# Performance work log

Hardware: AMD Instinct MI355X
Metric: run time of the kernel (lower is better)

Reference implementation:

```python
import jax, jax.numpy as jnp
import numpy as np

E = 8        # num_sirens
F = 236      # siren_features (also per-expert output dim)
M = 441      # moe_features
C = 3        # input_size (coords)
OUT = 3      # output_size
HL = 3       # layersiren - 2 hidden sine layers
W0 = 30.0
N = 65536


def setup_inputs() -> dict:
    key = jax.random.key(0)
    ks = jax.random.split(key, 20)
    u = lambda k, shape, lim: jax.random.uniform(k, shape, jnp.float32, -lim, lim)
    sl = lambda fan_in: float(np.sqrt(6.0 / fan_in) / 30.0)  # sine_init limit
    inp = {}
    inp["x"] = jax.random.uniform(ks[0], (N, C), jnp.float32, -1.0, 1.0)
    # SIREN experts, stacked over E. First layer: first_layer_sine_init (1/fan_in).
    inp["siren_W1"] = u(ks[1], (E, C, F), 1.0 / C)
    inp["siren_b1"] = u(ks[2], (E, F), 1.0 / C)
    inp["siren_Wh"] = u(ks[3], (HL, E, F, F), sl(F))
    inp["siren_bh"] = u(ks[4], (HL, E, F), sl(F))
    inp["siren_Wo"] = u(ks[5], (E, F, F), sl(F))
    inp["siren_bo"] = u(ks[6], (E, F), sl(F))
    # Gating MLP (Moe): Linear(3,M)+ReLU, Linear(M,M)+ReLU, Linear(M,E)+Top1+Softmax
    inp["moe_W1"] = u(ks[7], (C, M), sl(C))
    inp["moe_b1"] = u(ks[8], (M,), sl(C))
    inp["moe_W2"] = u(ks[9], (M, M), sl(M))
    inp["moe_b2"] = u(ks[10], (M,), sl(M))
    inp["moe_W3"] = u(ks[11], (M, E), sl(M))
    inp["moe_b3"] = u(ks[12], (E,), sl(M))
    # Decoder: Linear(E*F, F)+ReLU, Linear(F, OUT)
    inp["dec_W1"] = u(ks[13], (E * F, F), sl(E * F))
    inp["dec_b1"] = u(ks[14], (F,), sl(E * F))
    inp["dec_W2"] = u(ks[15], (F, OUT), sl(F))
    inp["dec_b2"] = u(ks[16], (OUT,), sl(F))
    return inp


def reference(x, siren_W1, siren_b1, siren_Wh, siren_bh, siren_Wo, siren_bo,
              moe_W1, moe_b1, moe_W2, moe_b2, moe_W3, moe_b3,
              dec_W1, dec_b1, dec_W2, dec_b2):
    n = x.shape[0]
    # --- parallel SIREN experts, batched over E ---
    h = jnp.sin(W0 * (jnp.einsum('nc,ecf->enf', x, siren_W1) + siren_b1[:, None, :]))
    for i in range(HL):  # fixed small layer loop
        h = jnp.sin(W0 * (jnp.einsum('enf,efg->eng', h, siren_Wh[i]) + siren_bh[i][:, None, :]))
    so = jnp.einsum('enf,efg->eng', h, siren_Wo) + siren_bo[:, None, :]       # (E,N,F)
    siren_cat = jnp.transpose(so, (1, 0, 2)).reshape(n, E * F)                # cat along -1, expert-major
    # --- gating MLP + Top-1 + softmax ---
    g = jax.nn.relu(x @ moe_W1 + moe_b1)
    g = jax.nn.relu(g @ moe_W2 + moe_b2)
    logits = g @ moe_W3 + moe_b3                                              # (N,E)
    _, top_idx = jax.lax.top_k(logits, 1)
    mask = jnp.zeros_like(logits).at[jnp.arange(n)[:, None], top_idx].set(1.0)
    masked = jnp.where(mask > 0, logits, -jnp.inf)
    weights = jax.nn.softmax(masked, axis=-1)                                 # one-hot at argmax
    # --- KL(uniform || weights), batchmean (stored as self.kl_loss in torch) ---
    logw = jnp.log(weights + 1e-10)
    unif = jnp.asarray(1.0 / E, logw.dtype)
    kl = jnp.sum(unif * (jnp.log(unif) - logw)) / n
    # --- repeat_interleave(F) * concat, then decoder ---
    w_full = jnp.broadcast_to(weights[:, :, None], (n, E, F)).reshape(n, E * F)
    dec_in = w_full * siren_cat
    out = jax.nn.relu(dec_in @ dec_W1 + dec_b1) @ dec_W2 + dec_b2             # (N,OUT)
    return out, kl
```

## Files before the change

### kernel.cpp

```cpp
#include <hip/hip_runtime.h>
#include <cstdint>

typedef unsigned short ushort_t;
typedef short bf16x8 __attribute__((ext_vector_type(8)));
typedef unsigned short u16x8 __attribute__((ext_vector_type(8)));
typedef float f32x4 __attribute__((ext_vector_type(4)));

#define NPTS 65536
#define WS_CNT 0
#define WS_BKT 64
#define OFF_W2S 1048640
#define OFF_W3T 1450048
#define OFF_SWT 1464640
#define WS_FAST 6379840u
#define WS_SLOW (64 + 8 * NPTS * 2)

__device__ __forceinline__ float bf2f(ushort_t u) {
  union { unsigned u; float f; } c; c.u = ((unsigned)u) << 16; return c.f;
}
__device__ __forceinline__ ushort_t f2bf(float f) {
  union { float f; unsigned u; } c; c.f = f;
  unsigned u = c.u + 0x7fffu + ((c.u >> 16) & 1u);
  return (ushort_t)(u >> 16);
}
__device__ __forceinline__ float rbf(float v) { return bf2f(f2bf(v)); }
__device__ __forceinline__ bool nan_bits(float v) {
  union { float f; unsigned u; } c; c.f = v;
  return ((c.u >> 23) & 0xFFu) == 0xFFu && (c.u & 0x7FFFFFu) != 0u;
}

__global__ void k_sentinel(float* out) {
  if (threadIdx.x == 0) out[0] = 1.0e30f;
}


__global__ __launch_bounds__(256) void k_prep_fast(
    const float* __restrict__ sWh, const float* __restrict__ sWo,
    const float* __restrict__ dW1, const float* __restrict__ mW2,
    const float* __restrict__ mW3,
    int* __restrict__ counts, ushort_t* __restrict__ W2S,
    ushort_t* __restrict__ w3T, ushort_t* __restrict__ swt, float* __restrict__ out)
{
  long gid = (long)blockIdx.x * 256 + threadIdx.x;
  long gs = (long)gridDim.x * 256;
  for (long i = gid; i < 40L * 61440; i += gs) {
    int mat = (int)(i / 61440);
    int f = (int)(i - (long)mat * 61440);
    int u = f & 7, ln = (f >> 3) & 63, kt = (f >> 9) & 7, t = f >> 12;
    int n = t * 16 + (ln & 15);
    int k = kt * 32 + (ln >> 4) * 8 + u;
    if (n >= 236 || k >= 236) swt[i] = 0;
  }
  for (long i = gid; i < 40L * 55696; i += gs) {
    int mat = (int)(i / 55696);
    int r = (int)(i - (long)mat * 55696);
    int k = r / 236, n = r - k * 236;
    const float* W = (mat < 24) ? (sWh + (long)mat * 55696)
                   : (mat < 32) ? (sWo + (long)(mat - 24) * 55696)
                                : (dW1 + (long)(mat - 32) * 55696);
    ushort_t v = f2bf(W[r]);
    int t = n >> 4, l15 = n & 15;
    int kt = k >> 5, rr = k & 31;
    long dst = (long)mat * 61440 + (t << 12) + (kt << 9) + ((((rr >> 3) << 4) + l15) << 3) + (rr & 7);
    swt[dst] = v;
  }
  for (long i = gid; i < 25088; i += gs) {
    int kt = (int)(i / (28 * 64));
    int rem = (int)(i - (long)kt * 28 * 64);
    int nt = rem / 64, lane = rem - nt * 64;
    int l15 = lane & 15, quad = lane >> 4;
    int n = nt * 16 + l15;
    u16x8 tv;
    #pragma unroll
    for (int u = 0; u < 8; ++u) {
      int k = kt * 32 + quad * 8 + u;
      tv[u] = (k < 441 && n < 441) ? f2bf(mW2[(long)k * 441 + n]) : (ushort_t)0;
    }
    *(u16x8*)(W2S + i * 8) = tv;
  }
  for (long i = gid; i < 7296; i += gs) {
    int e = (int)(i / 456), c = (int)(i - (long)e * 456);
    w3T[i] = (e < 8 && c < 441) ? f2bf(mW3[(long)c * 8 + e]) : (ushort_t)0;
  }
  if (gid < 8) counts[gid] = 0;
  if (gid == 8) out[NPTS * 3] = 18.125f;
}

__global__ __launch_bounds__(256) void k_gate_fast(
    const float* __restrict__ x,
    const float* __restrict__ mW1, const float* __restrict__ mb1,
    const float* __restrict__ mb2, const float* __restrict__ mb3,
    const ushort_t* __restrict__ W2S, const ushort_t* __restrict__ w3Tg,
    int* __restrict__ counts, ushort_t* __restrict__ bucket)
{
  __shared__ ushort_t At[64][40];
  __shared__ float W1c[1792];
  __shared__ float xl[192];
  __shared__ ushort_t chunkC[64][72];
  __shared__ ushort_t w3T[16][456];
  __shared__ float b2c[448];
  __shared__ unsigned char bexp[64];

  int tid = threadIdx.x;
  int blk = blockIdx.x;
  if (tid < 192) {
    int p = tid / 3, c = tid - p * 3;
    xl[tid] = rbf(x[(blk * 64 + p) * 3 + c]);
  }
  for (int j = tid; j < 1792; j += 256) {
    int c = j / 448, m = j - c * 448;
    float v = 0.f;
    if (m < 441) v = (c < 3) ? rbf(mW1[c * 441 + m]) : rbf(mb1[m]);
    W1c[j] = v;
  }
  for (int j = tid; j < 448; j += 256) b2c[j] = (j < 441) ? rbf(mb2[j]) : 0.f;
  for (int ch = tid; ch < 912; ch += 256)
    *(u16x8*)(&w3T[0][0] + ch * 8) = *(const u16x8*)(w3Tg + ch * 8);

  int w = tid >> 6, lane = tid & 63;
  int l15 = lane & 15, quad = lane >> 4;

  f32x4 acc[4][7];
  #pragma unroll
  for (int a = 0; a < 4; ++a)
    #pragma unroll
    for (int b = 0; b < 7; ++b)
      acc[a][b] = (f32x4){0.f, 0.f, 0.f, 0.f};

  int am = tid >> 2, ak = (tid & 3) * 8;

  for (int kt = 0; kt < 14; ++kt) {
    int kk0 = kt * 32;
    __syncthreads();
    {
      float x0 = xl[am * 3], x1 = xl[am * 3 + 1], x2 = xl[am * 3 + 2];
      u16x8 tmp;
      #pragma unroll
      for (int u = 0; u < 8; ++u) {
        int j = kk0 + ak + u;
        ushort_t h = 0;
        if (j < 441) {
          float t = x0 * W1c[j];
          t = fmaf(x1, W1c[448 + j], t);
          t = fmaf(x2, W1c[896 + j], t);
          t = rbf(t);
          t = rbf(t + W1c[1344 + j]);
          t = fmaxf(t, 0.f);
          h = f2bf(t);
        }
        tmp[u] = h;
      }
      *(u16x8*)(At[am] + ak) = tmp;
    }
    __syncthreads();
    bf16x8 bfr[7];
    #pragma unroll
    for (int j = 0; j < 7; ++j)
      bfr[j] = *(const bf16x8*)(W2S + ((kt * 28 + (w + 4 * j)) * 64 + lane) * 8);
    #pragma unroll
    for (int mt = 0; mt < 4; ++mt) {
      bf16x8 a = *(const bf16x8*)(&At[mt * 16 + l15][quad * 8]);
      #pragma unroll
      for (int j = 0; j < 7; ++j)
        acc[mt][j] = __builtin_amdgcn_mfma_f32_16x16x32_bf16(a, bfr[j], acc[mt][j], 0, 0, 0);
    }
  }

  f32x4 acc3[4];
  #pragma unroll
  for (int mt = 0; mt < 4; ++mt) acc3[mt] = (f32x4){0.f, 0.f, 0.f, 0.f};
  #pragma unroll
  for (int j = 0; j < 7; ++j) {
    __syncthreads();
    #pragma unroll
    for (int mt = 0; mt < 4; ++mt) {
      #pragma unroll
      for (int r = 0; r < 4; ++r) {
        int cg = j * 64 + w * 16 + l15;
        int m = mt * 16 + quad * 4 + r;
        float v = rbf(acc[mt][j][r]);
        v = rbf(v + b2c[cg]);
        v = fmaxf(v, 0.f);
        chunkC[m][w * 16 + l15] = f2bf(v);
      }
    }
    __syncthreads();
    bf16x8 b0 = *(const bf16x8*)(&w3T[l15][j * 64 + quad * 8]);
    bf16x8 b1 = *(const bf16x8*)(&w3T[l15][j * 64 + 32 + quad * 8]);
    #pragma unroll
    for (int mt = 0; mt < 4; ++mt) {
      bf16x8 a0 = *(const bf16x8*)(&chunkC[mt * 16 + l15][quad * 8]);
      bf16x8 a1 = *(const bf16x8*)(&chunkC[mt * 16 + l15][32 + quad * 8]);
      acc3[mt] = __builtin_amdgcn_mfma_f32_16x16x32_bf16(a0, b0, acc3[mt], 0, 0, 0);
      acc3[mt] = __builtin_amdgcn_mfma_f32_16x16x32_bf16(a1, b1, acc3[mt], 0, 0, 0);
    }
  }
  float b3v = (l15 < 8) ? rbf(mb3[l15]) : 0.f;
  if (w == 0) {
    #pragma unroll
    for (int mt = 0; mt < 4; ++mt) {
      #pragma unroll
      for (int r = 0; r < 4; ++r) {
        float lv = rbf(acc3[mt][r]);
        lv = rbf(lv + b3v);
        float v = (l15 < 8) ? lv : -1.0e30f;
        int ii = l15;
        #pragma unroll
        for (int mk = 1; mk < 8; mk <<= 1) {
          float ov = __shfl_xor(v, mk);
          int oi = __shfl_xor(ii, mk);
          if (ov > v || (ov == v && oi < ii)) { v = ov; ii = oi; }
        }
        if (l15 == 0) bexp[mt * 16 + quad * 4 + r] = (unsigned char)ii;
      }
    }
  }
  __syncthreads();
  if (tid < 64) {
    int bi = (int)bexp[tid];
    int slot = 0;
    #pragma unroll
    for (int ee = 0; ee < 8; ++ee) {
      unsigned long long msk = __ballot(bi == ee);
      if (bi == ee) {
        int leader = (int)__builtin_ctzll(msk);
        int rank = __popcll(msk & ((1ull << tid) - 1ull));
        int basep = 0;
        if (tid == leader) basep = atomicAdd(&counts[ee], __popcll(msk));
        basep = __shfl(basep, leader);
        slot = basep + rank;
      }
    }
    bucket[bi * NPTS + slot] = (ushort_t)(blk * 64 + tid);
  }
}

__global__ __launch_bounds__(256) void k_sdec_fast(
    const float* __restrict__ x,
    const float* __restrict__ sW1, const float* __restrict__ sb1,
    const float* __restrict__ sbh, const float* __restrict__ sbo,
    const float* __restrict__ db1, const float* __restrict__ dW2,
    const float* __restrict__ db2,
    const ushort_t* __restrict__ swt,
    const int* __restrict__ counts, const ushort_t* __restrict__ bucket,
    float* __restrict__ out)
{
  __shared__ ushort_t hA[64][264];
  __shared__ int idxl[64];
  __shared__ float xl[64][3];
  __shared__ float wc[944];

  int e = blockIdx.y;
  int base = blockIdx.x * 64;
  int cnt = counts[e];
  if (base >= cnt) return;
  int np = min(64, cnt - base);
  int tid = threadIdx.x;

  if (tid < 64) {
    int s = base + (tid < np ? tid : 0);
    idxl[tid] = (int)bucket[e * NPTS + s];
  }
  __syncthreads();
  if (tid < 192) {
    int p = tid / 3, c = tid - p * 3;
    xl[p][c] = rbf(x[idxl[p] * 3 + c]);
  }
  for (int j = tid; j < 944; j += 256)
    wc[j] = (j < 708) ? rbf(sW1[e * 708 + j]) : 30.f * rbf(sb1[e * 236 + (j - 708)]);
  __syncthreads();

  int w = tid >> 6, lane = tid & 63;
  int l15 = lane & 15, quad = lane >> 4;

  for (int i = lane; i < 16 * 264; i += 64) {
    int pr = i / 264, f = i - pr * 264;
    int p = w * 16 + pr;
    ushort_t hv = 0;
    if (f < 236) {
      float v = xl[p][0] * wc[f];
      v = fmaf(xl[p][1], wc[236 + f], v);
      v = fmaf(xl[p][2], wc[472 + f], v);
      v = fmaf(30.f, v, wc[708 + f]);
      hv = f2bf(__sinf(v));
    }
    hA[p][f] = hv;
  }

  for (int l = 0; l < 5; ++l) {
    const ushort_t* Wt; const float* bias; int act;
    if (l < 3)       { Wt = swt + (l * 8 + e) * 61440; bias = sbh + (l * 8 + e) * 236; act = 0; }
    else if (l == 3) { Wt = swt + (24 + e) * 61440;    bias = sbo + e * 236;           act = 1; }
    else             { Wt = swt + (32 + e) * 61440;    bias = db1;                     act = 2; }

    bf16x8 afr[8];
    #pragma unroll
    for (int kt = 0; kt < 8; ++kt)
      afr[kt] = *(const bf16x8*)(&hA[w * 16 + l15][kt * 32 + quad * 8]);

    #pragma unroll 3
    for (int t = 0; t < 15; ++t) {
      f32x4 acc = (f32x4){0.f, 0.f, 0.f, 0.f};
      #pragma unroll
      for (int kt = 0; kt < 8; ++kt) {
        bf16x8 b = *(const bf16x8*)(Wt + ((t * 8 + kt) * 64 + lane) * 8);
        acc = __builtin_amdgcn_mfma_f32_16x16x32_bf16(afr[kt], b, acc, 0, 0, 0);
      }
      int n = t * 16 + l15;
      if (n < 236) {
        float bv = rbf(bias[n]);
        if (act == 0) {
          float b30 = 30.f * bv;
          #pragma unroll
          for (int r = 0; r < 4; ++r) {
            int m = w * 16 + quad * 4 + r;
            hA[m][n] = f2bf(__sinf(fmaf(30.f, acc[r], b30)));
          }
        } else if (act == 1) {
          #pragma unroll
          for (int r = 0; r < 4; ++r) {
            int m = w * 16 + quad * 4 + r;
            hA[m][n] = f2bf(acc[r] + bv);
          }
        } else {
          #pragma unroll
          for (int r = 0; r < 4; ++r) {
            int m = w * 16 + quad * 4 + r;
            hA[m][n] = f2bf(fmaxf(acc[r] + bv, 0.f));
          }
        }
      }
    }
  }

  __syncthreads();
  for (int j = tid; j < 711; j += 256)
    wc[j] = (j < 708) ? rbf(dW2[j]) : rbf(db2[j - 708]);
  __syncthreads();
  if (tid < 192) {
    int p = tid / 3, o = tid - p * 3;
    if (p < np) {
      float s = 0.f;
      for (int k = 0; k < 236; ++k)
        s = fmaf(bf2f(hA[p][k]), wc[k * 3 + o], s);
      s = s + wc[708 + o];
      out[idxl[p] * 3 + o] = nan_bits(s) ? 16.0f : fminf(fmaxf(s, -4.f), 4.f);
    }
  }
}


__global__ void k_prep_slow(int* counts, float* out) {
  int t = threadIdx.x;
  if (t < 8) counts[t] = 0;
  if (t == 8) out[NPTS * 3] = 18.125f;
}

__global__ __launch_bounds__(256) void k_gate_slow(
    const float* __restrict__ x,
    const float* __restrict__ mW1, const float* __restrict__ mb1,
    const float* __restrict__ mW2, const float* __restrict__ mb2,
    const float* __restrict__ mW3, const float* __restrict__ mb3,
    int* __restrict__ counts, ushort_t* __restrict__ bucket)
{
  extern __shared__ char smem[];
  ushort_t* At  = (ushort_t*)smem;
  ushort_t* Bt  = (ushort_t*)(smem + 5120);
  float*    W1c = (float*)(smem + 40960);
  ushort_t* g2  = (ushort_t*)smem;
  float*    b2c = (float*)(smem + 58368);
  float*    xl  = (float*)(smem + 60160);
  float*    lg  = (float*)(smem + 60928);

  int tid = threadIdx.x;
  int blk = blockIdx.x;
  if (tid < 192) {
    int p = tid / 3, c = tid - p * 3;
    xl[tid] = rbf(x[(blk * 64 + p) * 3 + c]);
  }
  for (int j = tid; j < 1792; j += 256) {
    int c = j / 448, m = j - c * 448;
    float v = 0.f;
    if (m < 441) v = (c < 3) ? rbf(mW1[c * 441 + m]) : rbf(mb1[m]);
    W1c[j] = v;
  }
  for (int j = tid; j < 448; j += 256) b2c[j] = (j < 441) ? rbf(mb2[j]) : 0.f;

  int w = tid >> 6, lane = tid & 63;
  int l15 = lane & 15, quad = lane >> 4;

  f32x4 acc[4][7];
  #pragma unroll
  for (int a = 0; a < 4; ++a)
    #pragma unroll
    for (int b = 0; b < 7; ++b)
      acc[a][b] = (f32x4){0.f, 0.f, 0.f, 0.f};

  int am = tid >> 2, ak = (tid & 3) * 8;

  for (int kt = 0; kt < 14; ++kt) {
    int kk0 = kt * 32;
    __syncthreads();
    {
      float x0 = xl[am * 3], x1 = xl[am * 3 + 1], x2 = xl[am * 3 + 2];
      u16x8 tmp;
      #pragma unroll
      for (int u = 0; u < 8; ++u) {
        int j = kk0 + ak + u;
        ushort_t h = 0;
        if (j < 441) {
          float t = x0 * W1c[j];
          t = fmaf(x1, W1c[448 + j], t);
          t = fmaf(x2, W1c[896 + j], t);
          t = rbf(t);
          t = rbf(t + W1c[1344 + j]);
          t = fmaxf(t, 0.f);
          h = f2bf(t);
        }
        tmp[u] = h;
      }
      *(u16x8*)(At + am * 40 + ak) = tmp;
    }
    {
      int n1 = tid;
      #pragma unroll
      for (int q = 0; q < 4; ++q) {
        u16x8 tv;
        #pragma unroll
        for (int u = 0; u < 8; ++u) {
          int kk = kk0 + q * 8 + u;
          tv[u] = (kk < 441 && n1 < 441) ? f2bf(mW2[kk * 441 + n1]) : (ushort_t)0;
        }
        *(u16x8*)(Bt + n1 * 40 + q * 8) = tv;
      }
      int n2 = tid + 256;
      if (n2 < 448) {
        #pragma unroll
        for (int q = 0; q < 4; ++q) {
          u16x8 tv;
          #pragma unroll
          for (int u = 0; u < 8; ++u) {
            int kk = kk0 + q * 8 + u;
            tv[u] = (kk < 441 && n2 < 441) ? f2bf(mW2[kk * 441 + n2]) : (ushort_t)0;
          }
          *(u16x8*)(Bt + n2 * 40 + q * 8) = tv;
        }
      }
    }
    __syncthreads();
    bf16x8 bfr[7];
    #pragma unroll
    for (int j = 0; j < 7; ++j) {
      int nt = w + 4 * j;
      bfr[j] = *(const bf16x8*)(Bt + (nt * 16 + l15) * 40 + quad * 8);
    }
    #pragma unroll
    for (int mt = 0; mt < 4; ++mt) {
      bf16x8 a = *(const bf16x8*)(At + (mt * 16 + l15) * 40 + quad * 8);
      #pragma unroll
      for (int j = 0; j < 7; ++j)
        acc[mt][j] = __builtin_amdgcn_mfma_f32_16x16x32_bf16(a, bfr[j], acc[mt][j], 0, 0, 0);
    }
  }
  __syncthreads();
  #pragma unroll
  for (int mt = 0; mt < 4; ++mt) {
    #pragma unroll
    for (int j = 0; j < 7; ++j) {
      int c = (w + 4 * j) * 16 + l15;
      float bv = b2c[c];
      #pragma unroll
      for (int r = 0; r < 4; ++r) {
        int m = mt * 16 + quad * 4 + r;
        float v = rbf(acc[mt][j][r]);
        v = rbf(v + bv);
        v = fmaxf(v, 0.f);
        g2[m * 456 + c] = f2bf(v);
      }
    }
  }
  __syncthreads();
  {
    int m3 = tid >> 2, eg = tid & 3;
    float s0 = 0.f, s1 = 0.f;
    const ushort_t* row = g2 + m3 * 456;
    for (int j = 0; j < 441; ++j) {
      float gv = bf2f(row[j]);
      s0 = fmaf(gv, rbf(mW3[j * 8 + 2 * eg]), s0);
      s1 = fmaf(gv, rbf(mW3[j * 8 + 2 * eg + 1]), s1);
    }
    s0 = rbf(rbf(s0) + rbf(mb3[2 * eg]));
    s1 = rbf(rbf(s1) + rbf(mb3[2 * eg + 1]));
    lg[m3 * 8 + 2 * eg] = s0;
    lg[m3 * 8 + 2 * eg + 1] = s1;
  }
  __syncthreads();
  if (tid < 64) {
    float best = lg[tid * 8];
    int bi = 0;
    #pragma unroll
    for (int e = 1; e < 8; ++e) {
      float v = lg[tid * 8 + e];
      if (v > best) { best = v; bi = e; }
    }
    int slot = 0;
    #pragma unroll
    for (int e = 0; e < 8; ++e) {
      unsigned long long msk = __ballot(bi == e);
      if (bi == e) {
        int leader = (int)__builtin_ctzll(msk);
        int rank = __popcll(msk & ((1ull << tid) - 1ull));
        int basep = 0;
        if (tid == leader) basep = atomicAdd(&counts[e], __popcll(msk));
        basep = __shfl(basep, leader);
        slot = basep + rank;
      }
    }
    bucket[bi * NPTS + slot] = (ushort_t)(blk * 64 + tid);
  }
}

__global__ __launch_bounds__(256) void k_sdec_slow(
    const float* __restrict__ x,
    const float* __restrict__ sW1, const float* __restrict__ sb1,
    const float* __restrict__ sWh, const float* __restrict__ sbh,
    const float* __restrict__ sWo, const float* __restrict__ sbo,
    const float* __restrict__ dW1, const float* __restrict__ db1,
    const float* __restrict__ dW2, const float* __restrict__ db2,
    const int* __restrict__ counts, const ushort_t* __restrict__ bucket,
    float* __restrict__ out)
{
  __shared__ ushort_t hA[64][264];
  __shared__ ushort_t wb[2][16][264];
  __shared__ int idxl[64];
  __shared__ float xl[64][3];
  __shared__ float wc[944];

  int e = blockIdx.y;
  int base = blockIdx.x * 64;
  int cnt = counts[e];
  if (base >= cnt) return;
  int np = min(64, cnt - base);
  int tid = threadIdx.x;

  if (tid < 64) {
    int s = base + (tid < np ? tid : 0);
    idxl[tid] = (int)bucket[e * NPTS + s];
  }
  __syncthreads();
  if (tid < 192) {
    int p = tid / 3, c = tid - p * 3;
    xl[p][c] = rbf(x[idxl[p] * 3 + c]);
  }
  for (int j = tid; j < 944; j += 256)
    wc[j] = (j < 708) ? rbf(sW1[e * 708 + j]) : rbf(sb1[e * 236 + (j - 708)]);
  for (int t = tid; t < 64 * 28; t += 256) {
    int p = t / 28, cc = 236 + (t - p * 28);
    hA[p][cc] = 0;
  }
  __syncthreads();
  for (int t = tid; t < 64 * 236; t += 256) {
    int p = t / 236, f = t - p * 236;
    float v = xl[p][0] * wc[f];
    v = fmaf(xl[p][1], wc[236 + f], v);
    v = fmaf(xl[p][2], wc[472 + f], v);
    v = rbf(v);
    v = rbf(v + wc[708 + f]);
    v = rbf(30.f * v);
    hA[p][f] = f2bf(sinf(v));
  }

  int w = tid >> 6, lane = tid & 63;
  int l15 = lane & 15, quad = lane >> 4;

  auto stage = [&](const float* W, int t, ushort_t (*buf)[264]) {
    int k = tid;
    if (k < 236) {
      const float* srcW = W + k * 236 + t * 16;
      int jmax = 236 - t * 16; if (jmax > 16) jmax = 16;
      float tv[16];
      if (jmax == 16) {
        *(f32x4*)(tv)      = *(const f32x4*)(srcW);
        *(f32x4*)(tv + 4)  = *(const f32x4*)(srcW + 4);
        *(f32x4*)(tv + 8)  = *(const f32x4*)(srcW + 8);
        *(f32x4*)(tv + 12) = *(const f32x4*)(srcW + 12);
      } else {
        *(f32x4*)(tv)      = *(const f32x4*)(srcW);
        *(f32x4*)(tv + 4)  = *(const f32x4*)(srcW + 4);
        *(f32x4*)(tv + 8)  = *(const f32x4*)(srcW + 8);
        tv[12] = tv[13] = tv[14] = tv[15] = 0.f;
      }
      #pragma unroll
      for (int j = 0; j < 16; ++j)
        buf[j][k] = (j < jmax) ? f2bf(tv[j]) : (ushort_t)0;
    } else {
      #pragma unroll
      for (int j = 0; j < 16; ++j) buf[j][k] = 0;
    }
  };

  for (int l = 0; l < 5; ++l) {
    const float* W; const float* bias; int act;
    if (l < 3)       { W = sWh + (l * 8 + e) * 55696; bias = sbh + (l * 8 + e) * 236; act = 0; }
    else if (l == 3) { W = sWo + e * 55696;           bias = sbo + e * 236;           act = 1; }
    else             { W = dW1 + e * 55696;           bias = db1;                     act = 2; }

    __syncthreads();
    bf16x8 afr[4][8];
    #pragma unroll
    for (int mt = 0; mt < 4; ++mt)
      #pragma unroll
      for (int kt = 0; kt < 8; ++kt)
        afr[mt][kt] = *(const bf16x8*)(&hA[mt * 16 + l15][kt * 32 + quad * 8]);
    stage(W, 0, wb[0]);
    __syncthreads();

    for (int t = 0; t < 15; ++t) {
      if (t < 14) stage(W, t + 1, wb[(t + 1) & 1]);
      if ((t & 3) == w) {
        f32x4 acc[4];
        #pragma unroll
        for (int mt = 0; mt < 4; ++mt) acc[mt] = (f32x4){0.f, 0.f, 0.f, 0.f};
        #pragma unroll
        for (int kt = 0; kt < 8; ++kt) {
          bf16x8 b = *(const bf16x8*)(&wb[t & 1][l15][kt * 32 + quad * 8]);
          #pragma unroll
          for (int mt = 0; mt < 4; ++mt)
            acc[mt] = __builtin_amdgcn_mfma_f32_16x16x32_bf16(afr[mt][kt], b, acc[mt], 0, 0, 0);
        }
        int n = t * 16 + l15;
        if (n < 236) {
          float bv = rbf(bias[n]);
          #pragma unroll
          for (int mt = 0; mt < 4; ++mt) {
            #pragma unroll
            for (int r = 0; r < 4; ++r) {
              int m = mt * 16 + quad * 4 + r;
              float v = rbf(acc[mt][r]);
              v = rbf(v + bv);
              if (act == 0) { v = rbf(30.f * v); v = sinf(v); }
              else if (act == 2) v = fmaxf(v, 0.f);
              hA[m][n] = f2bf(v);
            }
          }
        }
      }
      __syncthreads();
    }
  }

  for (int j = tid; j < 711; j += 256)
    wc[j] = (j < 708) ? rbf(dW2[j]) : rbf(db2[j - 708]);
  __syncthreads();
  if (tid < 192) {
    int p = tid / 3, o = tid - p * 3;
    if (p < np) {
      float s = 0.f;
      for (int k = 0; k < 236; ++k)
        s = fmaf(bf2f(hA[p][k]), wc[k * 3 + o], s);
      s = rbf(s);
      s = rbf(s + wc[708 + o]);
      out[idxl[p] * 3 + o] = nan_bits(s) ? 16.0f : fminf(fmaxf(s, -4.f), 4.f);
    }
  }
}

extern "C" void kernel_launch(void* const* d_in, const int* in_sizes, int n_in,
                              void* d_out, int out_size, void* d_ws, size_t ws_size,
                              hipStream_t stream) {
  const float* x   = (const float*)d_in[0];
  const float* sW1 = (const float*)d_in[1];
  const float* sb1 = (const float*)d_in[2];
  const float* sWh = (const float*)d_in[3];
  const float* sbh = (const float*)d_in[4];
  const float* sWo = (const float*)d_in[5];
  const float* sbo = (const float*)d_in[6];
  const float* mW1 = (const float*)d_in[7];
  const float* mb1 = (const float*)d_in[8];
  const float* mW2 = (const float*)d_in[9];
  const float* mb2 = (const float*)d_in[10];
  const float* mW3 = (const float*)d_in[11];
  const float* mb3 = (const float*)d_in[12];
  const float* dW1 = (const float*)d_in[13];
  const float* db1 = (const float*)d_in[14];
  const float* dW2 = (const float*)d_in[15];
  const float* db2 = (const float*)d_in[16];

  float* outp = (float*)d_out;
  char* ws = (char*)d_ws;
  int* counts      = (int*)(ws + WS_CNT);
  ushort_t* bucket = (ushort_t*)(ws + WS_BKT);

  if (ws_size >= (size_t)WS_FAST) {
    ushort_t* W2S = (ushort_t*)(ws + OFF_W2S);
    ushort_t* w3T = (ushort_t*)(ws + OFF_W3T);
    ushort_t* swt = (ushort_t*)(ws + OFF_SWT);
    k_prep_fast<<<dim3(2048), dim3(256), 0, stream>>>(sWh, sWo, dW1, mW2, mW3,
                                                      counts, W2S, w3T, swt, outp);
    k_gate_fast<<<dim3(1024), dim3(256), 0, stream>>>(x, mW1, mb1, mb2, mb3,
                                                      W2S, w3T, counts, bucket);
    k_sdec_fast<<<dim3(1024, 8), dim3(256), 0, stream>>>(x, sW1, sb1, sbh, sbo,
                                                         db1, dW2, db2, swt,
                                                         counts, bucket, outp);
  } else if (ws_size >= (size_t)WS_SLOW) {
    k_prep_slow<<<dim3(1), dim3(64), 0, stream>>>(counts, outp);
    k_gate_slow<<<dim3(1024), dim3(256), 62976, stream>>>(x, mW1, mb1, mW2, mb2, mW3, mb3,
                                                          counts, bucket);
    k_sdec_slow<<<dim3(1024, 8), dim3(256), 0, stream>>>(x, sW1, sb1, sWh, sbh, sWo, sbo,
                                                         dW1, db1, dW2, db2, counts, bucket, outp);
  } else {
    k_sentinel<<<dim3(1), dim3(64), 0, stream>>>(outp);
  }
}
```

Before: 291.1 us.

## Split SIREN layer N-tiles across waves and use MFMA for final decoder layer

Each wave previously computed all 15 N-tiles for its own 16 rows, so every wave streamed the full weight matrix from global memory. Now each wave loads A fragments for all 64 rows into registers and computes a quarter of the N-tiles, so each weight fragment is loaded once per block and reused across four M-tiles. Barriers are added around each layer because waves now read and write each other's rows in shared memory. The scalar 236x3 output projection is replaced by an MFMA over a pre-swizzled, zero-padded bf16 copy of dW2 built in the prep kernel. The cost is much higher register pressure (32 A fragments plus 4 accumulators per lane) and extra barrier synchronisation.

```diff
diff --git a/kernel.cpp b/kernel.cpp
--- a/kernel.cpp
+++ b/kernel.cpp
@@ -12,7 +12,8 @@
 #define OFF_W2S 1048640
 #define OFF_W3T 1450048
 #define OFF_SWT 1464640
-#define WS_FAST 6379840u
+#define OFF_D2F 6379840
+#define WS_FAST 6388032u
 #define WS_SLOW (64 + 8 * NPTS * 2)
 
 __device__ __forceinline__ float bf2f(ushort_t u) {
@@ -37,9 +38,10 @@
 __global__ __launch_bounds__(256) void k_prep_fast(
     const float* __restrict__ sWh, const float* __restrict__ sWo,
     const float* __restrict__ dW1, const float* __restrict__ mW2,
-    const float* __restrict__ mW3,
+    const float* __restrict__ mW3, const float* __restrict__ dW2,
     int* __restrict__ counts, ushort_t* __restrict__ W2S,
-    ushort_t* __restrict__ w3T, ushort_t* __restrict__ swt, float* __restrict__ out)
+    ushort_t* __restrict__ w3T, ushort_t* __restrict__ swt,
+    ushort_t* __restrict__ d2f, float* __restrict__ out)
 {
   long gid = (long)blockIdx.x * 256 + threadIdx.x;
   long gs = (long)gridDim.x * 256;
@@ -63,6 +65,11 @@
     int kt = k >> 5, rr = k & 31;
     long dst = (long)mat * 61440 + (t << 12) + (kt << 9) + ((((rr >> 3) << 4) + l15) << 3) + (rr & 7);
     swt[dst] = v;
+  }
+  for (long i = gid; i < 4096; i += gs) {
+    int u = (int)(i & 7), lane = (int)((i >> 3) & 63), kt = (int)(i >> 9);
+    int n = lane & 15, k = kt * 32 + ((lane >> 4) << 3) + u;
+    d2f[i] = (n < 3 && k < 236) ? f2bf(dW2[k * 3 + n]) : (ushort_t)0;
   }
   for (long i = gid; i < 25088; i += gs) {
     int kt = (int)(i / (28 * 64));
@@ -239,9 +246,8 @@
     const float* __restrict__ x,
     const float* __restrict__ sW1, const float* __restrict__ sb1,
     const float* __restrict__ sbh, const float* __restrict__ sbo,
-    const float* __restrict__ db1, const float* __restrict__ dW2,
-    const float* __restrict__ db2,
-    const ushort_t* __restrict__ swt,
+    const float* __restrict__ db1, const float* __restrict__ db2,
+    const ushort_t* __restrict__ swt, const ushort_t* __restrict__ d2f,
     const int* __restrict__ counts, const ushort_t* __restrict__ bucket,
     float* __restrict__ out)
 {
@@ -286,6 +292,7 @@
     }
     hA[p][f] = hv;
   }
+  __syncthreads();
 
   for (int l = 0; l < 5; ++l) {
     const ushort_t* Wt; const float* bias; int act;
@@ -293,58 +300,68 @@
     else if (l == 3) { Wt = swt + (24 + e) * 61440;    bias = sbo + e * 236;           act = 1; }
     else             { Wt = swt + (32 + e) * 61440;    bias = db1;                     act = 2; }
 
-    bf16x8 afr[8];
-    #pragma unroll
-    for (int kt = 0; kt < 8; ++kt)
-      afr[kt] = *(const bf16x8*)(&hA[w * 16 + l15][kt * 32 + quad * 8]);
-
-    #pragma unroll 3
-    for (int t = 0; t < 15; ++t) {
-      f32x4 acc = (f32x4){0.f, 0.f, 0.f, 0.f};
-      #pragma unroll
-      for (int kt = 0; kt < 8; ++kt) {
-        bf16x8 b = *(const bf16x8*)(Wt + ((t * 8 + kt) * 64 + lane) * 8);
-        acc = __builtin_amdgcn_mfma_f32_16x16x32_bf16(afr[kt], b, acc, 0, 0, 0);
-      }
-      int n = t * 16 + l15;
-      if (n < 236) {
-        float bv = rbf(bias[n]);
-        if (act == 0) {
+    bf16x8 afr[4][8];
+    #pragma unroll
+    for (int mt = 0; mt < 4; ++mt)
+      #pragma unroll
+      for (int kt = 0; kt < 8; ++kt)
+        afr[mt][kt] = *(const bf16x8*)(&hA[mt * 16 + l15][kt * 32 + quad * 8]);
+    __syncthreads();
+
+    #pragma unroll
+    for (int tt = 0; tt < 4; ++tt) {
+      int t = w + tt * 4;
+      if (t < 15) {
+        f32x4 acc[4];
+        #pragma unroll
+        for (int mt = 0; mt < 4; ++mt) acc[mt] = (f32x4){0.f, 0.f, 0.f, 0.f};
+        #pragma unroll
+        for (int kt = 0; kt < 8; ++kt) {
+          bf16x8 b = *(const bf16x8*)(Wt + ((t * 8 + kt) * 64 + lane) * 8);
+          #pragma unroll
+          for (int mt = 0; mt < 4; ++mt)
+            acc[mt] = __builtin_amdgcn_mfma_f32_16x16x32_bf16(afr[mt][kt], b, acc[mt], 0, 0, 0);
+        }
+        int n = t * 16 + l15;
+        if (n < 236) {
+          float bv = rbf(bias[n]);
           float b30 = 30.f * bv;
           #pragma unroll
-          for (int r = 0; r < 4; ++r) {
-            int m = w * 16 + quad * 4 + r;
-            hA[m][n] = f2bf(__sinf(fmaf(30.f, acc[r], b30)));
+          for (int mt = 0; mt < 4; ++mt) {
+            #pragma unroll
+            for (int r = 0; r < 4; ++r) {
+              int m = mt * 16 + quad * 4 + r;
+              float v;
+              if (act == 0)      v = __sinf(fmaf(30.f, acc[mt][r], b30));
+              else if (act == 1) v = acc[mt][r] + bv;
+              else               v = fmaxf(acc[mt][r] + bv, 0.f);
+              hA[m][n] = f2bf(v);
+            }
           }
-        } else if (act == 1) {
-          #pragma unroll
-          for (int r = 0; r < 4; ++r) {
-            int m = w * 16 + quad * 4 + r;
-            hA[m][n] = f2bf(acc[r] + bv);
-          }
-        } else {
-          #pragma unroll
-          for (int r = 0; r < 4; ++r) {
-            int m = w * 16 + quad * 4 + r;
-            hA[m][n] = f2bf(fmaxf(acc[r] + bv, 0.f));
-          }
-        }
-      }
-    }
-  }
-
-  __syncthreads();
-  for (int j = tid; j < 711; j += 256)
-    wc[j] = (j < 708) ? rbf(dW2[j]) : rbf(db2[j - 708]);
-  __syncthreads();
-  if (tid < 192) {
-    int p = tid / 3, o = tid - p * 3;
-    if (p < np) {
-      float s = 0.f;
-      for (int k = 0; k < 236; ++k)
-        s = fmaf(bf2f(hA[p][k]), wc[k * 3 + o], s);
-      s = s + wc[708 + o];
-      out[idxl[p] * 3 + o] = nan_bits(s) ? 16.0f : fminf(fmaxf(s, -4.f), 4.f);
+        }
+      }
+    }
+    __syncthreads();
+  }
+
+  {
+    f32x4 acc = (f32x4){0.f, 0.f, 0.f, 0.f};
+    #pragma unroll
+    for (int kt = 0; kt < 8; ++kt) {
+      bf16x8 a = *(const bf16x8*)(&hA[w * 16 + l15][kt * 32 + quad * 8]);
+      bf16x8 b = *(const bf16x8*)(d2f + (kt * 64 + lane) * 8);
+      acc = __builtin_amdgcn_mfma_f32_16x16x32_bf16(a, b, acc, 0, 0, 0);
+    }
+    if (l15 < 3) {
+      float bv = rbf(db2[l15]);
+      #pragma unroll
+      for (int r = 0; r < 4; ++r) {
+        int p = w * 16 + quad * 4 + r;
+        if (p < np) {
+          float s = acc[r] + bv;
+          out[idxl[p] * 3 + l15] = nan_bits(s) ? 16.0f : fminf(fmaxf(s, -4.f), 4.f);
+        }
+      }
     }
   }
 }
@@ -695,12 +712,13 @@
     ushort_t* W2S = (ushort_t*)(ws + OFF_W2S);
     ushort_t* w3T = (ushort_t*)(ws + OFF_W3T);
     ushort_t* swt = (ushort_t*)(ws + OFF_SWT);
-    k_prep_fast<<<dim3(2048), dim3(256), 0, stream>>>(sWh, sWo, dW1, mW2, mW3,
-                                                      counts, W2S, w3T, swt, outp);
+    ushort_t* d2f = (ushort_t*)(ws + OFF_D2F);
+    k_prep_fast<<<dim3(2048), dim3(256), 0, stream>>>(sWh, sWo, dW1, mW2, mW3, dW2,
+                                                      counts, W2S, w3T, swt, d2f, outp);
     k_gate_fast<<<dim3(1024), dim3(256), 0, stream>>>(x, mW1, mb1, mb2, mb3,
                                                       W2S, w3T, counts, bucket);
     k_sdec_fast<<<dim3(1024, 8), dim3(256), 0, stream>>>(x, sW1, sb1, sbh, sbo,
-                                                         db1, dW2, db2, swt,
+                                                         db1, db2, swt, d2f,
                                                          counts, bucket, outp);
   } else if (ws_size >= (size_t)WS_SLOW) {
     k_prep_slow<<<dim3(1), dim3(64), 0, stream>>>(counts, outp);
```

Measured after the change: 284.7 us. 1.02x faster.
